# Kernel optimization log

Measured on AMD Instinct MI355X. Metric: run time of the kernel, lower is better.

## Reference

```python
import jax, jax.numpy as jnp
import numpy as np

PAD = 4  # DrQv2 random-shift padding


def setup_inputs() -> dict:
    key = jax.random.key(0)
    k1, k2 = jax.random.split(key)
    B, L, c, h, w = 32, 16, 9, 84, 84
    x = jax.random.normal(k1, (B, L, c, h, w), dtype=jnp.float32)
    # per-image integer pixel shifts in [0, 2*pad], column 0 = x-shift, column 1 = y-shift
    shift = jax.random.randint(k2, (B * L, 2), 0, 2 * PAD + 1, dtype=jnp.int32)
    return {"x": x, "shift": shift}


def reference(x, shift):
    # x: [B, L, c, h, w] (channels_first=True); shift: [(B*L), 2] int (sx, sy)
    B, L, c, h, w = x.shape
    xf = x.reshape(B * L, c, h, w)
    # replicate pad, same as F.pad(..., 'replicate')
    padded = jnp.pad(xf, ((0, 0), (0, 0), (PAD, PAD), (PAD, PAD)), mode="edge")
    # The base grid samples exact pixel centers of the padded image and the
    # random shift is an integer number of pixels, so bilinear grid_sample
    # reduces exactly to a shifted crop of the padded buffer:
    # out[b, :, i, j] = padded[b, :, i + sy, j + sx]
    def crop(img, s):
        return jax.lax.dynamic_slice(img, (0, s[1], s[0]), (c, h, w))

    out = jax.vmap(crop)(padded, shift)  # [(B*L), c, h, w]
    return out.reshape(B, L, c, h, w)
```

## Files before the change

### kernel.cpp

```cpp
#include <hip/hip_runtime.h>
#include <type_traits>


#define PAD 4

constexpr int CC     = 9;
constexpr int H      = 84;
constexpr int W      = 84;
constexpr int PLANE  = H * W;
constexpr int PLANE4 = PLANE / 4;
constexpr int W4     = W / 4;
constexpr int NBLK   = 512 * CC;

__global__ __launch_bounds__(256, 4)
void drq_aug_kernel(const float* __restrict__ x,
                    const int*   __restrict__ shift,
                    float*       __restrict__ out)
{
    const int blk = blockIdx.x;
    const int b   = blk / CC;
    const int dx  = shift[2 * b]     - PAD;
    const int dy  = shift[2 * b + 1] - PAD;
    const int qoff = dx >> 2;
    const int rot  = dx & 3;

    const float4* __restrict__ src4 = (const float4*)(x   + (size_t)blk * PLANE);
    float4*       __restrict__ dst4 = (float4*)      (out + (size_t)blk * PLANE);

    const int tid = threadIdx.x;

    float4 A[7], B[7];
    int    c0_[7];
    bool   act[7];

    #pragma unroll
    for (int rr = 0; rr < 7; ++rr) {
        int p  = rr * 256 + tid;
        act[rr] = (p < PLANE4);
        int pc = act[rr] ? p : PLANE4 - 1;
        int i  = pc / W4;
        int j4 = pc - i * W4;
        int si = i + dy;  si = si < 0 ? 0 : (si > H - 1 ? H - 1 : si);
        int q  = j4 + qoff;
        int q0 = q < 0 ? 0 : (q > W4 - 1 ? W4 - 1 : q);
        int q1 = q + 1;
        q1 = q1 < 0 ? 0 : (q1 > W4 - 1 ? W4 - 1 : q1);
        const float4* __restrict__ row4 = src4 + si * W4;
        A[rr] = row4[q0];
        B[rr] = row4[q1];
        c0_[rr] = (j4 << 2) + dx;
    }

    auto body = [&](auto rotc) {
        constexpr int R = decltype(rotc)::value;
        #pragma unroll
        for (int rr = 0; rr < 7; ++rr) {
            float4 a = A[rr], bb = B[rr];
            float4 v;
            if constexpr (R == 0)      v = a;
            else if constexpr (R == 1) v = make_float4(a.y, a.z, a.w, bb.x);
            else if constexpr (R == 2) v = make_float4(a.z, a.w, bb.x, bb.y);
            else                       v = make_float4(a.w, bb.x, bb.y, bb.z);
            int c0 = c0_[rr];
            if (dx < 0) {
                v.x = (c0     < 0) ? a.x : v.x;
                v.y = (c0 + 1 < 0) ? a.x : v.y;
                v.z = (c0 + 2 < 0) ? a.x : v.z;
                v.w = (c0 + 3 < 0) ? a.x : v.w;
            } else if (dx > 0) {
                v.x = (c0     > W - 1) ? bb.w : v.x;
                v.y = (c0 + 1 > W - 1) ? bb.w : v.y;
                v.z = (c0 + 2 > W - 1) ? bb.w : v.z;
                v.w = (c0 + 3 > W - 1) ? bb.w : v.w;
            }
            if (act[rr]) dst4[rr * 256 + tid] = v;
        }
    };

    switch (rot) {
        case 0:  body(std::integral_constant<int, 0>{}); break;
        case 1:  body(std::integral_constant<int, 1>{}); break;
        case 2:  body(std::integral_constant<int, 2>{}); break;
        default: body(std::integral_constant<int, 3>{}); break;
    }
}

extern "C" void kernel_launch(void* const* d_in, const int* in_sizes, int n_in,
                              void* d_out, int out_size, void* d_ws, size_t ws_size,
                              hipStream_t stream)
{
    const float* x     = (const float*)d_in[0];
    const int*   shift = (const int*)d_in[1];
    float*       out   = (float*)d_out;

    drq_aug_kernel<<<NBLK, 256, 0, stream>>>(x, shift, out);
}
```

Measured before the change: 228.8 us.

## Split each plane across seven blocks and use nontemporal stores

Each 84x84 plane was handled by one block looping over seven float4 chunks per thread. Now each chunk gets its own block, giving seven times more blocks with one float4 output per thread. Output is written with nontemporal stores so the streaming writes do not pollute the cache. More blocks can hide memory latency better, but they also add launch and per-block overhead, and many threads in the last sub-block sit idle.

```diff
diff --git a/kernel.cpp b/kernel.cpp
--- a/kernel.cpp
+++ b/kernel.cpp
@@ -10,71 +10,67 @@
 constexpr int PLANE  = H * W;
 constexpr int PLANE4 = PLANE / 4;
 constexpr int W4     = W / 4;
-constexpr int NBLK   = 512 * CC;
+constexpr int SUBS   = 7;
+constexpr int NBLK   = 512 * CC * SUBS;
 
-__global__ __launch_bounds__(256, 4)
+typedef float vf4 __attribute__((ext_vector_type(4)));
+
+__global__ __launch_bounds__(256)
 void drq_aug_kernel(const float* __restrict__ x,
                     const int*   __restrict__ shift,
                     float*       __restrict__ out)
 {
-    const int blk = blockIdx.x;
-    const int b   = blk / CC;
-    const int dx  = shift[2 * b]     - PAD;
-    const int dy  = shift[2 * b + 1] - PAD;
+    const int bid   = blockIdx.x;
+    const int plane = bid / SUBS;
+    const int sub   = bid - plane * SUBS;
+
+    const int p = sub * 256 + (int)threadIdx.x;
+    if (p >= PLANE4) return;
+
+    const int b  = plane / CC;
+    const int dx = shift[2 * b]     - PAD;
+    const int dy = shift[2 * b + 1] - PAD;
     const int qoff = dx >> 2;
     const int rot  = dx & 3;
 
-    const float4* __restrict__ src4 = (const float4*)(x   + (size_t)blk * PLANE);
-    float4*       __restrict__ dst4 = (float4*)      (out + (size_t)blk * PLANE);
+    const float4* __restrict__ src4 = (const float4*)(x   + (size_t)plane * PLANE);
+    float*        __restrict__ dstf = out + (size_t)plane * PLANE;
 
-    const int tid = threadIdx.x;
+    const int i  = p / W4;
+    const int j4 = p - i * W4;
+    int si = i + dy;  si = si < 0 ? 0 : (si > H - 1 ? H - 1 : si);
 
-    float4 A[7], B[7];
-    int    c0_[7];
-    bool   act[7];
+    int q  = j4 + qoff;
+    int q0 = q < 0 ? 0 : (q > W4 - 1 ? W4 - 1 : q);
+    int q1 = q + 1;
+    q1 = q1 < 0 ? 0 : (q1 > W4 - 1 ? W4 - 1 : q1);
 
-    #pragma unroll
-    for (int rr = 0; rr < 7; ++rr) {
-        int p  = rr * 256 + tid;
-        act[rr] = (p < PLANE4);
-        int pc = act[rr] ? p : PLANE4 - 1;
-        int i  = pc / W4;
-        int j4 = pc - i * W4;
-        int si = i + dy;  si = si < 0 ? 0 : (si > H - 1 ? H - 1 : si);
-        int q  = j4 + qoff;
-        int q0 = q < 0 ? 0 : (q > W4 - 1 ? W4 - 1 : q);
-        int q1 = q + 1;
-        q1 = q1 < 0 ? 0 : (q1 > W4 - 1 ? W4 - 1 : q1);
-        const float4* __restrict__ row4 = src4 + si * W4;
-        A[rr] = row4[q0];
-        B[rr] = row4[q1];
-        c0_[rr] = (j4 << 2) + dx;
-    }
+    const float4* __restrict__ row4 = src4 + si * W4;
+    const float4 a  = row4[q0];
+    const float4 bb = row4[q1];
+
+    const int c0 = (j4 << 2) + dx;
 
     auto body = [&](auto rotc) {
         constexpr int R = decltype(rotc)::value;
-        #pragma unroll
-        for (int rr = 0; rr < 7; ++rr) {
-            float4 a = A[rr], bb = B[rr];
-            float4 v;
-            if constexpr (R == 0)      v = a;
-            else if constexpr (R == 1) v = make_float4(a.y, a.z, a.w, bb.x);
-            else if constexpr (R == 2) v = make_float4(a.z, a.w, bb.x, bb.y);
-            else                       v = make_float4(a.w, bb.x, bb.y, bb.z);
-            int c0 = c0_[rr];
-            if (dx < 0) {
-                v.x = (c0     < 0) ? a.x : v.x;
-                v.y = (c0 + 1 < 0) ? a.x : v.y;
-                v.z = (c0 + 2 < 0) ? a.x : v.z;
-                v.w = (c0 + 3 < 0) ? a.x : v.w;
-            } else if (dx > 0) {
-                v.x = (c0     > W - 1) ? bb.w : v.x;
-                v.y = (c0 + 1 > W - 1) ? bb.w : v.y;
-                v.z = (c0 + 2 > W - 1) ? bb.w : v.z;
-                v.w = (c0 + 3 > W - 1) ? bb.w : v.w;
-            }
-            if (act[rr]) dst4[rr * 256 + tid] = v;
+        float4 v;
+        if constexpr (R == 0)      v = a;
+        else if constexpr (R == 1) v = make_float4(a.y, a.z, a.w, bb.x);
+        else if constexpr (R == 2) v = make_float4(a.z, a.w, bb.x, bb.y);
+        else                       v = make_float4(a.w, bb.x, bb.y, bb.z);
+        if (dx < 0) {
+            v.x = (c0     < 0) ? a.x : v.x;
+            v.y = (c0 + 1 < 0) ? a.x : v.y;
+            v.z = (c0 + 2 < 0) ? a.x : v.z;
+            v.w = (c0 + 3 < 0) ? a.x : v.w;
+        } else if (dx > 0) {
+            v.x = (c0     > W - 1) ? bb.w : v.x;
+            v.y = (c0 + 1 > W - 1) ? bb.w : v.y;
+            v.z = (c0 + 2 > W - 1) ? bb.w : v.z;
+            v.w = (c0 + 3 > W - 1) ? bb.w : v.w;
         }
+        vf4 nv = { v.x, v.y, v.z, v.w };
+        __builtin_nontemporal_store(nv, (vf4*)(dstf + 4 * p));
     };
 
     switch (rot) {
```

New measurement: 215.9 us. 1.06x faster.
